# Kernel tuning notes

Hardware: AMD Instinct MI355X
Metric: run time of the kernel (lower is better)

The kernel has to match this reference:

```python
import jax, jax.numpy as jnp
import numpy as np

N = 50000
E = 800000
D = 128
L = 3
EPS = 1e-5


def setup_inputs() -> dict:
    key = jax.random.key(0)
    ks = jax.random.split(key, 8)
    x = jax.random.normal(ks[0], (N, D), dtype=jnp.float32)
    edge_index = jax.random.randint(ks[1], (2, E), 0, N, dtype=jnp.int64)
    s = 1.0 / np.sqrt(D)
    # stacked per-layer params (all layers are 128->128)
    Wl = jax.random.uniform(ks[2], (L, D, D), jnp.float32, -s, s)  # lin_l weight
    bl = jax.random.uniform(ks[3], (L, D), jnp.float32, -s, s)     # lin_l bias
    Wr = jax.random.uniform(ks[4], (L, D, D), jnp.float32, -s, s)  # lin_r weight (no bias)
    gamma = jnp.ones((L, D), jnp.float32)
    beta = jnp.zeros((L, D), jnp.float32)
    return {"x": x, "edge_index": edge_index, "Wl": Wl, "bl": bl,
            "Wr": Wr, "gamma": gamma, "beta": beta}


def layer_norm(h, g, b):
    mu = jnp.mean(h, axis=-1, keepdims=True)
    var = jnp.mean(jnp.square(h - mu), axis=-1, keepdims=True)
    return (h - mu) * jax.lax.rsqrt(var + EPS) * g + b


def reference(x, edge_index, Wl, bl, Wr, gamma, beta):
    src = edge_index[0]
    dst = edge_index[1]
    # in-degree counts (constant wrt features)
    cnt = jax.ops.segment_sum(jnp.ones((E,), jnp.float32), dst, num_segments=N)
    inv_cnt = (1.0 / jnp.maximum(cnt, 1.0))[:, None]  # [N,1]
    h = x
    for l in range(L):
        # mean neighbor aggregation: gather source feats, scatter-add to dst
        agg = jax.ops.segment_sum(h[src], dst, num_segments=N) * inv_cnt
        # SAGEConv: lin_l(agg) + lin_r(h)
        h2 = agg @ Wl[l].T + bl[l] + h @ Wr[l].T
        h2 = layer_norm(h2, gamma[l], beta[l])
        h = jax.nn.relu(h2)  # dropout is identity at inference
    return h
```

## Files before the change

### kernel.cpp

```cpp
#include <hip/hip_runtime.h>
#include <hip/hip_bf16.h>
#include <stdint.h>

#define NN 50000
#define EE 800000
#define DD 128
#define LL 3
#define FILL_CHUNKS 196
#define FILL_PER 4096

typedef __attribute__((ext_vector_type(8))) short short8;
typedef __attribute__((ext_vector_type(4))) float float4v;

__device__ __forceinline__ float bf2f(unsigned int u) {
  union { unsigned int i; float f; } x; x.i = u << 16; return x.f;
}
__device__ __forceinline__ unsigned short f2bf(float f) {
  union { float f; unsigned int i; } x; x.f = f;
  unsigned int r = x.i + 0x7FFFu + ((x.i >> 16) & 1u);
  return (unsigned short)(r >> 16);
}

__global__ void deg_kernel(const int* __restrict__ dst, int* __restrict__ deg, int E) {
  int t = blockIdx.x * blockDim.x + threadIdx.x;
  int e = t * 4;
  if (e + 3 < E) {
    int4 d = *(const int4*)(dst + e);
    atomicAdd(&deg[d.x], 1);
    atomicAdd(&deg[d.y], 1);
    atomicAdd(&deg[d.z], 1);
    atomicAdd(&deg[d.w], 1);
  } else {
    for (int i = e; i < E; i++) atomicAdd(&deg[dst[i]], 1);
  }
}

__global__ __launch_bounds__(256) void scan1_kernel(
    const int* __restrict__ deg, int* __restrict__ incl, int* __restrict__ partial, int N) {
  __shared__ int wsums[4];
  const int tid = threadIdx.x, lane = tid & 63, wid = tid >> 6;
  int i = blockIdx.x * 256 + tid;
  int v = (i < N) ? deg[i] : 0;
  int x = v;
#pragma unroll
  for (int off = 1; off < 64; off <<= 1) {
    int y = __shfl_up(x, off, 64);
    if (lane >= off) x += y;
  }
  if (lane == 63) wsums[wid] = x;
  __syncthreads();
  if (tid == 0) {
    int a0 = wsums[0], a1 = wsums[1], a2 = wsums[2];
    wsums[0] = 0; wsums[1] = a0; wsums[2] = a0 + a1; wsums[3] = a0 + a1 + a2;
  }
  __syncthreads();
  int inc = wsums[wid] + x;
  if (i < N) incl[i] = inc;
  if (tid == 255) partial[blockIdx.x] = inc;
}

__global__ __launch_bounds__(256) void scan2_kernel(int* __restrict__ partial, int P) {
  __shared__ int wsums[4];
  const int tid = threadIdx.x, lane = tid & 63, wid = tid >> 6;
  int v = (tid < P) ? partial[tid] : 0;
  int x = v;
#pragma unroll
  for (int off = 1; off < 64; off <<= 1) {
    int y = __shfl_up(x, off, 64);
    if (lane >= off) x += y;
  }
  if (lane == 63) wsums[wid] = x;
  __syncthreads();
  if (tid == 0) {
    int a0 = wsums[0], a1 = wsums[1], a2 = wsums[2];
    wsums[0] = 0; wsums[1] = a0; wsums[2] = a0 + a1; wsums[3] = a0 + a1 + a2;
  }
  __syncthreads();
  int excl = wsums[wid] + x - v;
  if (tid < P) partial[tid] = excl;
}

__global__ __launch_bounds__(256) void scan3_kernel(
    const int* __restrict__ incl, const int* __restrict__ deg, const int* __restrict__ partial,
    int* __restrict__ rowptr, int* __restrict__ cursor, int N) {
  int i = blockIdx.x * 256 + threadIdx.x;
  if (i < N) {
    int rp = incl[i] - deg[i] + partial[blockIdx.x];
    rowptr[i] = rp;
    cursor[i] = rp;
  }
  if (i == 0) rowptr[N] = EE;
}

__global__ __launch_bounds__(256) void fill_kernel(
    const int* __restrict__ src, const int* __restrict__ dst,
    int* __restrict__ cursor, int* __restrict__ col, int E) {
  const int range = blockIdx.x & 7;
  const int chunk = blockIdx.x >> 3;
  const int lo = range * (NN / 8);
  const int hi = lo + (NN / 8);
  const int e0 = chunk * FILL_PER;
  const int e1 = (e0 + FILL_PER < E) ? (e0 + FILL_PER) : E;
  for (int eb = e0 + threadIdx.x * 4; eb < e1; eb += 256 * 4) {
    if (eb + 3 < e1) {
      int4 d4 = *(const int4*)(dst + eb);
      int dd[4] = {d4.x, d4.y, d4.z, d4.w};
      bool m[4];
      int sv[4], pos[4];
#pragma unroll
      for (int j = 0; j < 4; j++) m[j] = (dd[j] >= lo) & (dd[j] < hi);
#pragma unroll
      for (int j = 0; j < 4; j++) if (m[j]) sv[j] = src[eb + j];
#pragma unroll
      for (int j = 0; j < 4; j++) if (m[j]) pos[j] = atomicAdd(&cursor[dd[j]], 1);
#pragma unroll
      for (int j = 0; j < 4; j++) if (m[j]) col[pos[j]] = sv[j];
    } else {
      for (int e = eb; e < e1; e++) {
        int d = dst[e];
        if (d >= lo && d < hi) {
          int pos = atomicAdd(&cursor[d], 1);
          col[pos] = src[e];
        }
      }
    }
  }
}

__global__ void convert_kernel(const float* __restrict__ x, unsigned short* __restrict__ hbf, int n4) {
  int i = blockIdx.x * blockDim.x + threadIdx.x;
  if (i < n4) {
    float4 v = ((const float4*)x)[i];
    ushort4 o;
    o.x = f2bf(v.x); o.y = f2bf(v.y); o.z = f2bf(v.z); o.w = f2bf(v.w);
    ((ushort4*)hbf)[i] = o;
  }
}

__global__ void repack_kernel(const float* __restrict__ Wl, const float* __restrict__ Wr,
                              unsigned short* __restrict__ out) {
  int tid = blockIdx.x * blockDim.x + threadIdx.x;
  if (tid >= LL * 8 * 8 * 64) return;
  int lane = tid & 63;
  int t = (tid >> 6) & 7;
  int ks = (tid >> 9) & 7;
  int l = tid >> 12;
  int n = t * 16 + (lane & 15);
  int kbase = ks * 32 + (lane >> 4) * 8;
  const float* Wsrc = (ks < 4) ? (Wl + ((size_t)(l * 128 + n) * 128 + kbase))
                               : (Wr + ((size_t)(l * 128 + n) * 128 + (kbase - 128)));
#pragma unroll
  for (int j = 0; j < 8; j++) out[(size_t)tid * 8 + j] = f2bf(Wsrc[j]);
}

__global__ __launch_bounds__(256) void agg_kernel(
    const unsigned short* __restrict__ hbf, const int* __restrict__ rowptr,
    const int* __restrict__ col, unsigned short* __restrict__ agg, int N) {
  int node = blockIdx.x * 4 + (threadIdx.x >> 6);
  if (node >= N) return;
  int lane = threadIdx.x & 63;
  int s = rowptr[node], e = rowptr[node + 1];
  float ax = 0.f, ay = 0.f;
  int i = s;
  for (; i + 15 < e; i += 16) {
    int idx[16];
#pragma unroll
    for (int j = 0; j < 16; j++) idx[j] = col[i + j];
    unsigned int r[16];
#pragma unroll
    for (int j = 0; j < 16; j++) r[j] = ((const unsigned int*)(hbf + (size_t)idx[j] * 128))[lane];
#pragma unroll
    for (int j = 0; j < 16; j++) {
      ax += bf2f(r[j] & 0xffffu);
      ay += bf2f(r[j] >> 16);
    }
  }
  if (i + 7 < e) {
    int idx[8];
#pragma unroll
    for (int j = 0; j < 8; j++) idx[j] = col[i + j];
    unsigned int r[8];
#pragma unroll
    for (int j = 0; j < 8; j++) r[j] = ((const unsigned int*)(hbf + (size_t)idx[j] * 128))[lane];
#pragma unroll
    for (int j = 0; j < 8; j++) {
      ax += bf2f(r[j] & 0xffffu);
      ay += bf2f(r[j] >> 16);
    }
    i += 8;
  }
  if (i + 3 < e) {
    int idx[4];
#pragma unroll
    for (int j = 0; j < 4; j++) idx[j] = col[i + j];
    unsigned int r[4];
#pragma unroll
    for (int j = 0; j < 4; j++) r[j] = ((const unsigned int*)(hbf + (size_t)idx[j] * 128))[lane];
#pragma unroll
    for (int j = 0; j < 4; j++) {
      ax += bf2f(r[j] & 0xffffu);
      ay += bf2f(r[j] >> 16);
    }
    i += 4;
  }
  for (; i < e; i++) {
    unsigned int r0 = ((const unsigned int*)(hbf + (size_t)col[i] * 128))[lane];
    ax += bf2f(r0 & 0xffffu);
    ay += bf2f(r0 >> 16);
  }
  int dg = e - s;
  float inv = 1.0f / (float)(dg > 1 ? dg : 1);
  ax *= inv; ay *= inv;
  ((unsigned int*)(agg + (size_t)node * 128))[lane] =
      ((unsigned int)f2bf(ay) << 16) | (unsigned int)f2bf(ax);
}

template <bool LAST>
__global__ __launch_bounds__(256) void gemm_ln_mfma_kernel(
    const unsigned short* __restrict__ agg, const unsigned short* __restrict__ h,
    const unsigned short* __restrict__ Bf, const float* __restrict__ bias,
    const float* __restrict__ gamma, const float* __restrict__ beta,
    unsigned short* __restrict__ out_bf, float* __restrict__ f_out, int N) {
  __shared__ unsigned short Bl[8 * 8 * 512];
  __shared__ float reds[64][16];
  __shared__ float redss[64][16];
  __shared__ float mu_s[64], rs_s[64];
  const int tid = threadIdx.x;
  {
    const uint4* srcB = (const uint4*)Bf;
    uint4* dstB = (uint4*)Bl;
#pragma unroll
    for (int i = 0; i < 16; i++) dstB[tid + i * 256] = srcB[tid + i * 256];
  }
  __syncthreads();
  const int wave = tid >> 6, lane = tid & 63;
  const int ln16 = lane & 15, quad = lane >> 4;
  const int m0 = blockIdx.x * 64 + wave * 16;
  int row_a = m0 + ln16;
  if (row_a > N - 1) row_a = N - 1;
  const size_t aoff = (size_t)row_a * 128 + quad * 8;

  float4v acc[8];
#pragma unroll
  for (int t = 0; t < 8; t++) acc[t] = (float4v)0.f;

#pragma unroll
  for (int ks = 0; ks < 8; ks++) {
    const unsigned short* ap = (ks < 4) ? (agg + aoff + ks * 32) : (h + aoff + (ks - 4) * 32);
    short8 a = *(const short8*)ap;
#pragma unroll
    for (int t = 0; t < 8; t++) {
      short8 b = *(const short8*)&Bl[(ks * 8 + t) * 512 + lane * 8];
      acc[t] = __builtin_amdgcn_mfma_f32_16x16x32_bf16(a, b, acc[t], 0, 0, 0);
    }
  }

  float bias_v[8], g_v[8], b_v[8];
#pragma unroll
  for (int t = 0; t < 8; t++) {
    int c = t * 16 + ln16;
    bias_v[t] = bias[c]; g_v[t] = gamma[c]; b_v[t] = beta[c];
  }
#pragma unroll
  for (int r = 0; r < 4; r++) {
    float s = 0.f, ss = 0.f;
#pragma unroll
    for (int t = 0; t < 8; t++) {
      float val = acc[t][r] + bias_v[t];
      s += val; ss += val * val;
    }
    int rowblk = wave * 16 + quad * 4 + r;
    reds[rowblk][ln16] = s;
    redss[rowblk][ln16] = ss;
  }
  __syncthreads();
  if (tid < 64) {
    float s = 0.f, ss = 0.f;
#pragma unroll
    for (int g = 0; g < 16; g++) { s += reds[tid][g]; ss += redss[tid][g]; }
    float mu = s * (1.0f / 128.0f);
    float var = ss * (1.0f / 128.0f) - mu * mu;
    if (var < 0.f) var = 0.f;
    mu_s[tid] = mu;
    rs_s[tid] = rsqrtf(var + 1e-5f);
  }
  __syncthreads();
#pragma unroll
  for (int r = 0; r < 4; r++) {
    int row = m0 + quad * 4 + r;
    int rowblk = wave * 16 + quad * 4 + r;
    if (row < N) {
      float mu = mu_s[rowblk], rs = rs_s[rowblk];
#pragma unroll
      for (int t = 0; t < 8; t++) {
        float val = acc[t][r] + bias_v[t];
        float y = (val - mu) * rs * g_v[t] + b_v[t];
        y = y > 0.f ? y : 0.f;
        int cidx = t * 16 + ln16;
        if (LAST) {
          f_out[(size_t)row * 128 + cidx] = y;
        } else {
          out_bf[(size_t)row * 128 + cidx] = f2bf(y);
        }
      }
    }
  }
}

extern "C" void kernel_launch(void* const* d_in, const int* in_sizes, int n_in,
                              void* d_out, int out_size, void* d_ws, size_t ws_size,
                              hipStream_t stream) {
  const float* x = (const float*)d_in[0];
  const int* edge = (const int*)d_in[1];
  const float* Wl = (const float*)d_in[2];
  const float* bl = (const float*)d_in[3];
  const float* Wr = (const float*)d_in[4];
  const float* gamma = (const float*)d_in[5];
  const float* beta = (const float*)d_in[6];
  float* out = (float*)d_out;

  const int* srcv = edge;
  const int* dstv = edge + EE;

  char* p = (char*)d_ws;
  auto alloc = [&](size_t bytes) {
    char* r = p;
    p += (bytes + 255) & ~(size_t)255;
    return r;
  };
  const size_t bplane = (size_t)NN * 128 * 2;
  unsigned short* xB = (unsigned short*)alloc(bplane);
  unsigned short* h1B = (unsigned short*)alloc(bplane);
  unsigned short* h2B = (unsigned short*)alloc(bplane);
  unsigned short* agB = (unsigned short*)alloc(bplane);
  unsigned short* BfB = (unsigned short*)alloc((size_t)LL * 32768 * 2);
  int* deg = (int*)alloc((size_t)NN * 4);
  int* incl = (int*)alloc((size_t)NN * 4);
  int* cursor = (int*)alloc((size_t)NN * 4);
  int* rowptr = (int*)alloc((size_t)(NN + 1) * 4);
  int* colarr = (int*)alloc((size_t)EE * 4);
  int* partial = (int*)alloc((size_t)256 * 4);
  if ((size_t)(p - (char*)d_ws) > ws_size) return;

  const int SCAN_BLOCKS = (NN + 255) / 256;

  hipMemsetAsync(deg, 0, (size_t)NN * 4, stream);
  deg_kernel<<<(EE / 4 + 255) / 256, 256, 0, stream>>>(dstv, deg, EE);
  scan1_kernel<<<SCAN_BLOCKS, 256, 0, stream>>>(deg, incl, partial, NN);
  scan2_kernel<<<1, 256, 0, stream>>>(partial, SCAN_BLOCKS);
  scan3_kernel<<<SCAN_BLOCKS, 256, 0, stream>>>(incl, deg, partial, rowptr, cursor, NN);
  fill_kernel<<<8 * FILL_CHUNKS, 256, 0, stream>>>(srcv, dstv, cursor, colarr, EE);
  convert_kernel<<<(NN * 128 / 4 + 255) / 256, 256, 0, stream>>>(x, xB, NN * 128 / 4);
  repack_kernel<<<(LL * 4096 + 255) / 256, 256, 0, stream>>>(Wl, Wr, BfB);

  const int gemm_grid = (NN + 63) / 64;
  const int agg_grid = (NN + 3) / 4;

  agg_kernel<<<agg_grid, 256, 0, stream>>>(xB, rowptr, colarr, agB, NN);
  gemm_ln_mfma_kernel<false><<<gemm_grid, 256, 0, stream>>>(
      agB, xB, BfB, bl, gamma, beta, h1B, nullptr, NN);

  agg_kernel<<<agg_grid, 256, 0, stream>>>(h1B, rowptr, colarr, agB, NN);
  gemm_ln_mfma_kernel<false><<<gemm_grid, 256, 0, stream>>>(
      agB, h1B, BfB + 32768, bl + 128, gamma + 128, beta + 128, h2B, nullptr, NN);

  agg_kernel<<<agg_grid, 256, 0, stream>>>(h2B, rowptr, colarr, agB, NN);
  gemm_ln_mfma_kernel<true><<<gemm_grid, 256, 0, stream>>>(
      agB, h2B, BfB + 2 * 32768, bl + 256, gamma + 256, beta + 256, nullptr, out, NN);
}
```

Before: 308.9 us.

## Split aggregation into two feature-half passes and merge setup kernels

Aggregation now runs as two passes, one per 64-column half of the bf16 features. Each wavefront's quarter-groups gather a different neighbor with 8-byte loads, then the partial sums are combined with cross-lane shuffles. The aim is to shrink each pass's gather working set so it fits in cache better and to keep more loads in flight per wave. The degree count, fp32-to-bf16 conversion and weight repack are merged into one front kernel to save launches, and the fill kernel's chunk size is now derived from the edge count. The cost is reading the rowptr and col arrays twice and doing extra shuffle reductions.

```diff
diff --git a/kernel.cpp b/kernel.cpp
--- a/kernel.cpp
+++ b/kernel.cpp
@@ -7,7 +7,10 @@
 #define DD 128
 #define LL 3
 #define FILL_CHUNKS 196
-#define FILL_PER 4096
+
+#define DEG_BLOCKS 782
+#define CONV_BLOCKS 6250
+#define REPACK_BLOCKS 48
 
 typedef __attribute__((ext_vector_type(8))) short short8;
 typedef __attribute__((ext_vector_type(4))) float float4v;
@@ -21,17 +24,42 @@
   return (unsigned short)(r >> 16);
 }
 
-__global__ void deg_kernel(const int* __restrict__ dst, int* __restrict__ deg, int E) {
-  int t = blockIdx.x * blockDim.x + threadIdx.x;
-  int e = t * 4;
-  if (e + 3 < E) {
-    int4 d = *(const int4*)(dst + e);
-    atomicAdd(&deg[d.x], 1);
-    atomicAdd(&deg[d.y], 1);
-    atomicAdd(&deg[d.z], 1);
-    atomicAdd(&deg[d.w], 1);
+__global__ __launch_bounds__(256) void front_kernel(
+    const int* __restrict__ dst, int* __restrict__ deg,
+    const float* __restrict__ x, unsigned short* __restrict__ hbf,
+    const float* __restrict__ Wl, const float* __restrict__ Wr,
+    unsigned short* __restrict__ wout) {
+  const int b = blockIdx.x;
+  const int tid = threadIdx.x;
+  if (b < DEG_BLOCKS) {
+    int e = (b * 256 + tid) * 4;
+    if (e + 3 < EE) {
+      int4 d = *(const int4*)(dst + e);
+      atomicAdd(&deg[d.x], 1);
+      atomicAdd(&deg[d.y], 1);
+      atomicAdd(&deg[d.z], 1);
+      atomicAdd(&deg[d.w], 1);
+    } else {
+      for (int i = e; i < EE; i++) atomicAdd(&deg[dst[i]], 1);
+    }
+  } else if (b < DEG_BLOCKS + CONV_BLOCKS) {
+    int i = (b - DEG_BLOCKS) * 256 + tid;
+    float4 v = ((const float4*)x)[i];
+    ushort4 o;
+    o.x = f2bf(v.x); o.y = f2bf(v.y); o.z = f2bf(v.z); o.w = f2bf(v.w);
+    ((ushort4*)hbf)[i] = o;
   } else {
-    for (int i = e; i < E; i++) atomicAdd(&deg[dst[i]], 1);
+    int t0 = (b - DEG_BLOCKS - CONV_BLOCKS) * 256 + tid;
+    int lane = t0 & 63;
+    int t = (t0 >> 6) & 7;
+    int ks = (t0 >> 9) & 7;
+    int l = t0 >> 12;
+    int n = t * 16 + (lane & 15);
+    int kbase = ks * 32 + (lane >> 4) * 8;
+    const float* Wsrc = (ks < 4) ? (Wl + ((size_t)(l * 128 + n) * 128 + kbase))
+                                 : (Wr + ((size_t)(l * 128 + n) * 128 + (kbase - 128)));
+#pragma unroll
+    for (int j = 0; j < 8; j++) wout[(size_t)t0 * 8 + j] = f2bf(Wsrc[j]);
   }
 }
 
@@ -99,8 +127,9 @@
   const int chunk = blockIdx.x >> 3;
   const int lo = range * (NN / 8);
   const int hi = lo + (NN / 8);
-  const int e0 = chunk * FILL_PER;
-  const int e1 = (e0 + FILL_PER < E) ? (e0 + FILL_PER) : E;
+  const int per = (E + FILL_CHUNKS - 1) / FILL_CHUNKS;
+  const int e0 = chunk * per;
+  const int e1 = (e0 + per < E) ? (e0 + per) : E;
   for (int eb = e0 + threadIdx.x * 4; eb < e1; eb += 256 * 4) {
     if (eb + 3 < e1) {
       int4 d4 = *(const int4*)(dst + eb);
@@ -127,92 +156,57 @@
   }
 }
 
-__global__ void convert_kernel(const float* __restrict__ x, unsigned short* __restrict__ hbf, int n4) {
-  int i = blockIdx.x * blockDim.x + threadIdx.x;
-  if (i < n4) {
-    float4 v = ((const float4*)x)[i];
-    ushort4 o;
-    o.x = f2bf(v.x); o.y = f2bf(v.y); o.z = f2bf(v.z); o.w = f2bf(v.w);
-    ((ushort4*)hbf)[i] = o;
-  }
-}
-
-__global__ void repack_kernel(const float* __restrict__ Wl, const float* __restrict__ Wr,
-                              unsigned short* __restrict__ out) {
-  int tid = blockIdx.x * blockDim.x + threadIdx.x;
-  if (tid >= LL * 8 * 8 * 64) return;
-  int lane = tid & 63;
-  int t = (tid >> 6) & 7;
-  int ks = (tid >> 9) & 7;
-  int l = tid >> 12;
-  int n = t * 16 + (lane & 15);
-  int kbase = ks * 32 + (lane >> 4) * 8;
-  const float* Wsrc = (ks < 4) ? (Wl + ((size_t)(l * 128 + n) * 128 + kbase))
-                               : (Wr + ((size_t)(l * 128 + n) * 128 + (kbase - 128)));
-#pragma unroll
-  for (int j = 0; j < 8; j++) out[(size_t)tid * 8 + j] = f2bf(Wsrc[j]);
-}
-
-__global__ __launch_bounds__(256) void agg_kernel(
+template <int PASS>
+__global__ __launch_bounds__(256) void agg_half_kernel(
     const unsigned short* __restrict__ hbf, const int* __restrict__ rowptr,
     const int* __restrict__ col, unsigned short* __restrict__ agg, int N) {
   int node = blockIdx.x * 4 + (threadIdx.x >> 6);
   if (node >= N) return;
   int lane = threadIdx.x & 63;
+  const int qtr = lane >> 4;
+  const int l16 = lane & 15;
   int s = rowptr[node], e = rowptr[node + 1];
-  float ax = 0.f, ay = 0.f;
+  const unsigned short* base = hbf + PASS * 64;
+  float a0 = 0.f, a1 = 0.f, a2 = 0.f, a3 = 0.f;
   int i = s;
   for (; i + 15 < e; i += 16) {
-    int idx[16];
-#pragma unroll
-    for (int j = 0; j < 16; j++) idx[j] = col[i + j];
-    unsigned int r[16];
-#pragma unroll
-    for (int j = 0; j < 16; j++) r[j] = ((const unsigned int*)(hbf + (size_t)idx[j] * 128))[lane];
-#pragma unroll
-    for (int j = 0; j < 16; j++) {
-      ax += bf2f(r[j] & 0xffffu);
-      ay += bf2f(r[j] >> 16);
-    }
-  }
-  if (i + 7 < e) {
-    int idx[8];
-#pragma unroll
-    for (int j = 0; j < 8; j++) idx[j] = col[i + j];
-    unsigned int r[8];
-#pragma unroll
-    for (int j = 0; j < 8; j++) r[j] = ((const unsigned int*)(hbf + (size_t)idx[j] * 128))[lane];
-#pragma unroll
-    for (int j = 0; j < 8; j++) {
-      ax += bf2f(r[j] & 0xffffu);
-      ay += bf2f(r[j] >> 16);
-    }
-    i += 8;
-  }
-  if (i + 3 < e) {
     int idx[4];
 #pragma unroll
-    for (int j = 0; j < 4; j++) idx[j] = col[i + j];
-    unsigned int r[4];
-#pragma unroll
-    for (int j = 0; j < 4; j++) r[j] = ((const unsigned int*)(hbf + (size_t)idx[j] * 128))[lane];
+    for (int j = 0; j < 4; j++) idx[j] = col[i + 4 * j + qtr];
+    uint2 r[4];
+#pragma unroll
+    for (int j = 0; j < 4; j++) r[j] = ((const uint2*)(base + (size_t)idx[j] * 128))[l16];
 #pragma unroll
     for (int j = 0; j < 4; j++) {
-      ax += bf2f(r[j] & 0xffffu);
-      ay += bf2f(r[j] >> 16);
-    }
-    i += 4;
-  }
-  for (; i < e; i++) {
-    unsigned int r0 = ((const unsigned int*)(hbf + (size_t)col[i] * 128))[lane];
-    ax += bf2f(r0 & 0xffffu);
-    ay += bf2f(r0 >> 16);
-  }
+      a0 += bf2f(r[j].x & 0xffffu); a1 += bf2f(r[j].x >> 16);
+      a2 += bf2f(r[j].y & 0xffffu); a3 += bf2f(r[j].y >> 16);
+    }
+  }
+  for (; i + 3 < e; i += 4) {
+    int idx = col[i + qtr];
+    uint2 r = ((const uint2*)(base + (size_t)idx * 128))[l16];
+    a0 += bf2f(r.x & 0xffffu); a1 += bf2f(r.x >> 16);
+    a2 += bf2f(r.y & 0xffffu); a3 += bf2f(r.y >> 16);
+  }
+  int rem = e - i;
+  if (qtr < rem) {
+    int idx = col[i + qtr];
+    uint2 r = ((const uint2*)(base + (size_t)idx * 128))[l16];
+    a0 += bf2f(r.x & 0xffffu); a1 += bf2f(r.x >> 16);
+    a2 += bf2f(r.y & 0xffffu); a3 += bf2f(r.y >> 16);
+  }
+  a0 += __shfl_xor(a0, 16); a0 += __shfl_xor(a0, 32);
+  a1 += __shfl_xor(a1, 16); a1 += __shfl_xor(a1, 32);
+  a2 += __shfl_xor(a2, 16); a2 += __shfl_xor(a2, 32);
+  a3 += __shfl_xor(a3, 16); a3 += __shfl_xor(a3, 32);
   int dg = e - s;
   float inv = 1.0f / (float)(dg > 1 ? dg : 1);
-  ax *= inv; ay *= inv;
-  ((unsigned int*)(agg + (size_t)node * 128))[lane] =
-      ((unsigned int)f2bf(ay) << 16) | (unsigned int)f2bf(ax);
+  if (qtr == 0) {
+    uint2 o;
+    o.x = ((unsigned int)f2bf(a1 * inv) << 16) | (unsigned int)f2bf(a0 * inv);
+    o.y = ((unsigned int)f2bf(a3 * inv) << 16) | (unsigned int)f2bf(a2 * inv);
+    ((uint2*)(agg + (size_t)node * 128 + PASS * 64))[l16] = o;
+  }
 }
 
 template <bool LAST>
@@ -345,26 +339,28 @@
   const int SCAN_BLOCKS = (NN + 255) / 256;
 
   hipMemsetAsync(deg, 0, (size_t)NN * 4, stream);
-  deg_kernel<<<(EE / 4 + 255) / 256, 256, 0, stream>>>(dstv, deg, EE);
+  front_kernel<<<DEG_BLOCKS + CONV_BLOCKS + REPACK_BLOCKS, 256, 0, stream>>>(
+      dstv, deg, x, xB, Wl, Wr, BfB);
   scan1_kernel<<<SCAN_BLOCKS, 256, 0, stream>>>(deg, incl, partial, NN);
   scan2_kernel<<<1, 256, 0, stream>>>(partial, SCAN_BLOCKS);
   scan3_kernel<<<SCAN_BLOCKS, 256, 0, stream>>>(incl, deg, partial, rowptr, cursor, NN);
   fill_kernel<<<8 * FILL_CHUNKS, 256, 0, stream>>>(srcv, dstv, cursor, colarr, EE);
-  convert_kernel<<<(NN * 128 / 4 + 255) / 256, 256, 0, stream>>>(x, xB, NN * 128 / 4);
-  repack_kernel<<<(LL * 4096 + 255) / 256, 256, 0, stream>>>(Wl, Wr, BfB);
 
   const int gemm_grid = (NN + 63) / 64;
   const int agg_grid = (NN + 3) / 4;
 
-  agg_kernel<<<agg_grid, 256, 0, stream>>>(xB, rowptr, colarr, agB, NN);
+  agg_half_kernel<0><<<agg_grid, 256, 0, stream>>>(xB, rowptr, colarr, agB, NN);
+  agg_half_kernel<1><<<agg_grid, 256, 0, stream>>>(xB, rowptr, colarr, agB, NN);
   gemm_ln_mfma_kernel<false><<<gemm_grid, 256, 0, stream>>>(
       agB, xB, BfB, bl, gamma, beta, h1B, nullptr, NN);
 
-  agg_kernel<<<agg_grid, 256, 0, stream>>>(h1B, rowptr, colarr, agB, NN);
+  agg_half_kernel<0><<<agg_grid, 256, 0, stream>>>(h1B, rowptr, colarr, agB, NN);
+  agg_half_kernel<1><<<agg_grid, 256, 0, stream>>>(h1B, rowptr, colarr, agB, NN);
   gemm_ln_mfma_kernel<false><<<gemm_grid, 256, 0, stream>>>(
       agB, h1B, BfB + 32768, bl + 128, gamma + 128, beta + 128, h2B, nullptr, NN);
 
-  agg_kernel<<<agg_grid, 256, 0, stream>>>(h2B, rowptr, colarr, agB, NN);
+  agg_half_kernel<0><<<agg_grid, 256, 0, stream>>>(h2B, rowptr, colarr, agB, NN);
+  agg_half_kernel<1><<<agg_grid, 256, 0, stream>>>(h2B, rowptr, colarr, agB, NN);
   gemm_ln_mfma_kernel<true><<<gemm_grid, 256, 0, stream>>>(
       agB, h2B, BfB + 2 * 32768, bl + 256, gamma + 256, beta + 256, nullptr, out, NN);
 }
```

Result: slower. 354.9 us (+14.9%).
